# Optimization experiments

Hardware: AMD Instinct MI355X
Metric: run time of the kernel (lower is better)

The kernel has to match this reference:

```python
import jax, jax.numpy as jnp
import numpy as np

T_NO = 501          # refractory kernel length
COS_BASIS_NO = 30   # raised-cosine basis count
SCALE = 7.5
SHIFT = 1


def make_kern_basis():
    # kern_basis[i, t] = 0.5*cos(scale*log(t+shift+1e-7) - pi/2*i) + 0.5, zeroed outside [phi-pi, phi+pi]
    i = np.arange(COS_BASIS_NO, dtype=np.float64)[:, None]
    phi = 0.5 * np.pi * i
    x = np.arange(T_NO, dtype=np.float64)[None, :]
    raw = SCALE * np.log(x + SHIFT + 1e-7)
    basis = 0.5 * np.cos(raw - phi) + 0.5
    basis = np.where((raw < phi - np.pi) | (raw > phi + np.pi), 0.0, basis)
    return jnp.asarray(basis, jnp.float32)  # [30, T_NO]


def setup_inputs() -> dict:
    key = jax.random.key(0)
    ks = jax.random.split(key, 7)
    B, T = 64, 2048
    H_no = 5
    return {
        "V": jax.random.normal(ks[0], (B, T), jnp.float32),
        "D": jax.random.normal(ks[1], (B, T), jnp.float32),
        "w1": jax.random.normal(ks[2], (H_no, 2, 1), jnp.float32) * 0.5,   # Conv1d(2->H, k=1)
        "b1": jax.random.normal(ks[3], (H_no,), jnp.float32) * 0.1,
        "w2": jax.random.normal(ks[4], (1, H_no, 1), jnp.float32) * 0.5,   # Conv1d(H->1, k=1)
        "b2": jax.random.normal(ks[5], (1,), jnp.float32) * 0.1,
        "W_refract": jax.random.normal(ks[6], (COS_BASIS_NO,), jnp.float32) * 0.01,
    }


def reference(V, D, w1, b1, w2, b2, W_refract):
    B, T = V.shape
    kern_basis = make_kern_basis()
    refract_kern = jnp.flip(kern_basis.T @ W_refract)  # [T_NO], flipped as in torch

    # Ring-buffer alignment: sample at time s lives in column s % T_NO. At time t,
    # the original weights the window [t-T_NO, t-1] with refract_kern[0..T_NO-1]
    # (oldest -> kern[0]), i.e. column c gets weight refract_kern[(c - t) % T_NO].
    idx = (jnp.arange(T_NO)[None, :] - jnp.arange(T_NO)[:, None]) % T_NO
    kern_table = refract_kern[idx]  # [T_NO, T_NO]; kern_table[t % T_NO] is weights for step t

    # K_no=1, L_no=2 -> pointwise MLP: tanh(Conv1x1(2->H)) then Conv1x1(H->1)
    x = jnp.stack([V, D], axis=1)                                        # [B, 2, T]
    h = jnp.tanh(jnp.einsum('hc,bct->bht', w1[:, :, 0], x) + b1[None, :, None])
    nn_out = jnp.einsum('h,bht->bt', w2[0, :, 0], h) + b2[0]             # [B, T]

    key0 = jax.random.key(42)

    def step(carry, xs):
        ring, key = carry
        t, nn_t = xs                                   # nn_t: [B]
        key, sub = jax.random.split(key)
        p = t % T_NO
        refract = ring @ kern_table[p]                 # [B] sliding-window sum
        P_t = jax.nn.sigmoid(nn_t + refract)
        spike = jax.random.bernoulli(sub, P_t).astype(V.dtype)
        ring = ring.at[:, p].set(spike)                # overwrite slot that just expired
        return (ring, key), (spike, P_t)

    ring0 = jnp.zeros((B, T_NO), V.dtype)
    (_, _), (S_seq, P_seq) = jax.lax.scan(step, (ring0, key0), (jnp.arange(T), nn_out.T))
    S_out = S_seq.T  # [B, T]
    P_out = P_seq.T  # [B, T]
    return S_out, P_out
```

## Files before the change

### kernel.cpp

```cpp
#include <hip/hip_runtime.h>
#include <stdint.h>

typedef unsigned long long ull;

#define TT 2048

struct TF2 { uint32_t x, y; };

constexpr TF2 tf2x32(uint32_t k0, uint32_t k1, uint32_t x0, uint32_t x1) {
  uint32_t ks2 = k0 ^ k1 ^ 0x1BD11BDAu;
  x0 += k0; x1 += k1;
#define TFR_(r) x0 += x1; x1 = __builtin_rotateleft32(x1, r); x1 ^= x0;
  TFR_(13) TFR_(15) TFR_(26) TFR_(6)
  x0 += k1;  x1 += ks2 + 1u;
  TFR_(17) TFR_(29) TFR_(16) TFR_(24)
  x0 += ks2; x1 += k0 + 2u;
  TFR_(13) TFR_(15) TFR_(26) TFR_(6)
  x0 += k0;  x1 += k1 + 3u;
  TFR_(17) TFR_(29) TFR_(16) TFR_(24)
  x0 += k1;  x1 += ks2 + 4u;
  TFR_(13) TFR_(15) TFR_(26) TFR_(6)
  x0 += ks2; x1 += k0 + 5u;
#undef TFR_
  return {x0, x1};
}

struct Half_ { uint32_t a[1024]; uint32_t b[1024]; uint32_t k0, k1; };

constexpr Half_ make_half(uint32_t k0, uint32_t k1) {
  Half_ h{};
  for (int t = 0; t < 1024; ++t) {
    TF2 nk = tf2x32(k0, k1, 0u, 0u);
    TF2 sb = tf2x32(k0, k1, 0u, 1u);
    h.a[t] = sb.x; h.b[t] = sb.y;
    k0 = nk.x; k1 = nk.y;
  }
  h.k0 = k0; h.k1 = k1;
  return h;
}

namespace ckeys {
constexpr Half_ H0 = make_half(0u, 42u);
constexpr Half_ H1 = make_half(H0.k0, H0.k1);
}
__constant__ Half_ dH0 = ckeys::H0;
__constant__ Half_ dH1 = ckeys::H1;

__device__ __forceinline__ float tanh_xla(float x) {
#pragma clang fp contract(off)
  float ax = fabsf(x);
  float xc = fminf(fmaxf(x, -7.90531110763549805f), 7.90531110763549805f);
  float x2 = xc * xc;
  float p = fmaf(x2, -2.76076847742355e-16f, 2.00018790482477e-13f);
  p = fmaf(x2, p, -8.60467152213735e-11f);
  p = fmaf(x2, p, 5.12229709037114e-08f);
  p = fmaf(x2, p, 1.48572235717979e-05f);
  p = fmaf(x2, p, 6.37261928875436e-04f);
  p = fmaf(x2, p, 4.89352455891786e-03f);
  p = xc * p;
  float q = fmaf(x2, 1.19825839466702e-06f, 1.18534705686654e-04f);
  q = fmaf(x2, q, 2.26843463243900e-03f);
  q = fmaf(x2, q, 4.89352518554385e-03f);
  return (ax < 0.0004f) ? x : (p / q);
}

__device__ __forceinline__ float sig_ref(float z) {
#pragma clang fp contract(off)
  float e = (float)exp(-(double)z);
  return 1.0f / (1.0f + e);
}

__device__ __forceinline__ uint32_t ford(float f) {
  uint32_t x = __float_as_uint(f);
  return (x & 0x80000000u) ? ~x : (x | 0x80000000u);
}
__device__ __forceinline__ float fdec(uint32_t k) {
  uint32_t b = (k & 0x80000000u) ? (k & 0x7fffffffu) : ~k;
  return __uint_as_float(b);
}

__device__ float find_tau(float u) {
  if (!(u > 0.0f)) return -1.0e30f;
  double zg = log((double)u / (1.0 - (double)u));
  float zgf = (float)zg;
  zgf = fminf(fmaxf(zgf, -90.0f), 90.0f);
  uint32_t kc = ford(zgf);
  uint32_t klo = kc - 96u, khi = kc + 96u;
  if (!(sig_ref(fdec(klo)) <= u)) klo = ford(-95.0f);
  if (!(sig_ref(fdec(khi)) > u))  khi = ford(95.0f);
  while (khi - klo > 1u) {
    uint32_t km = klo + ((khi - klo) >> 1);
    if (sig_ref(fdec(km)) <= u) klo = km; else khi = km;
  }
  return fdec(klo);
}

__global__ void ap_pre_kernel(const float* __restrict__ V, const float* __restrict__ D,
                              const float* __restrict__ w1, const float* __restrict__ b1,
                              const float* __restrict__ w2, const float* __restrict__ b2,
                              const float* __restrict__ Wr,
                              float* __restrict__ zb, float* __restrict__ tauA,
                              float* __restrict__ rk, uint32_t* flags) {
#pragma clang fp contract(off)
  int tid = threadIdx.x;
  int blk = blockIdx.x;
  if (blk < 512) {
    int idx = blk * 256 + tid;
    int b = idx >> 11, t = idx & 2047;
    float v = V[idx], dd = D[idx];
    float acc = 0.f;
#pragma unroll
    for (int h = 0; h < 5; ++h) {
      float m = fmaf(w1[2 * h + 1], dd, w1[2 * h] * v) + b1[h];
      float th = tanh_xla(m);
      acc = (h == 0) ? (w2[0] * th) : fmaf(w2[h], th, acc);
    }
    float z0 = acc + b2[0];
    uint32_t ka = (t < 1024) ? dH0.a[t] : dH1.a[t - 1024];
    uint32_t kb = (t < 1024) ? dH0.b[t] : dH1.b[t - 1024];
    TF2 o = tf2x32(ka, kb, 0u, (uint32_t)b);
    uint32_t bits = o.x ^ o.y;
    float u = __uint_as_float((bits >> 9) | 0x3f800000u) - 1.0f;
    zb[t * 64 + b] = z0;
    tauA[t * 64 + b] = find_tau(u);
  } else if (blk < 514) {
    int d = (blk - 512) * 256 + tid;
    float val = 0.f;
    if (d >= 1 && d <= 501) {
      double raw = 7.5 * log((double)(d - 1) + 1.0 + 1e-7);
      float a = 0.f;
      for (int i = 0; i < 30; ++i) {
        double phi = (0.5 * 3.141592653589793) * (double)i;
        float bf;
        if (raw < phi - 3.141592653589793 || raw > phi + 3.141592653589793) bf = 0.f;
        else bf = (float)(0.5 * cos(raw - phi) + 0.5);
        a = fmaf(Wr[i], bf, a);
      }
      val = a;
    }
    rk[d] = val;
  } else {
    if (tid == 0) flags[0] = 0u;
    if (tid >= 1 && tid <= 64) {
      int c = tid - 1;
      flags[tid] = (c <= 4) ? 4u : 0u;
    }
  }
}

__global__ void __launch_bounds__(512, 1)
ap_main_kernel(float* __restrict__ zb, const float* __restrict__ tauA,
               const float* __restrict__ rk, float* __restrict__ zarr,
               ull* __restrict__ sw, uint32_t* flags) {
  __shared__ float lutS[20 * 256];
  __shared__ uint32_t snapL[16 * 64];
  __shared__ uint32_t snapA[16 * 64];
  __shared__ float comboL[64 * 64];
  __shared__ int winDone[8];
  __shared__ int progLds;
  __shared__ ull swL[384];
  __shared__ uint32_t colb[64 * 13];
  __shared__ float rkL[512];

  int tid = threadIdx.x;
  int lane = tid & 63;

  if (blockIdx.x == 0) {
    for (int e = tid; e < 20 * 256; e += 512) {
      int o = e >> 8, vb = e & 255;
      float s = 0.f;
      if (o < 10) {
        for (int i = 0; i < 8; ++i)
          if (vb & (1 << i)) s += rk[3 + 8 * o + i];
      } else {
        for (int i = 0; i < 8; ++i)
          if (vb & (1 << i)) s += rk[3 + 8 * o + 7 - i];
      }
      lutS[e] = s;
    }
    if (tid < 8) winDone[tid] = 0;
    if (tid == 0) progLds = 0;
    __syncthreads();

    int wv = tid >> 6;

    if (wv == 0) {
      float rk1 = rk[1], rk2 = rk[2];
      float zbR[2][16], tauR[2][16];
#pragma unroll
      for (int q = 0; q < 16; ++q) {
        zbR[0][q]  = zb[q * 64 + lane];
        tauR[0][q] = tauA[q * 64 + lane];
        zbR[1][q]  = zb[1024 + q * 64 + lane];
        tauR[1][q] = tauA[1024 + q * 64 + lane];
      }
      while (__hip_atomic_load(&winDone[0], __ATOMIC_ACQUIRE, __HIP_MEMORY_SCOPE_WORKGROUP) != 1)
        __builtin_amdgcn_s_sleep(1);
      float cpipe[2];
      cpipe[0] = comboL[0 * 64 + lane];
      cpipe[1] = comboL[1 * 64 + lane];
      float l[2][10];
#pragma unroll
      for (int k = 0; k < 10; ++k) { l[0][k] = 0.f; l[1][k] = 0.f; }
      uint32_t m0 = 0, m1 = 0, m2 = 0;
      float s1f = 0.f, s2f = 0.f;

      for (int wp = 0; wp < 64; ++wp) {
#pragma unroll
        for (int half = 0; half < 2; ++half) {
          int w = 2 * wp + half;
          if (w < 127) {
            int slot = (w + 1) & 7, gen = w + 2;
            while (__hip_atomic_load(&winDone[slot], __ATOMIC_ACQUIRE,
                                     __HIP_MEMORY_SCOPE_WORKGROUP) != gen)
              __builtin_amdgcn_s_sleep(1);
          }
          if (half == 0) {
            int c2 = (w + 2) >> 1;
            if (c2 >= 5 && c2 <= 63) {
              while ((int)__hip_atomic_load(&flags[1 + c2], __ATOMIC_ACQUIRE,
                                            __HIP_MEMORY_SCOPE_AGENT) < 4)
                __builtin_amdgcn_s_sleep(2);
            }
          }
          int wl = (w + 2 <= 127) ? (w + 2) : 127;
          const float* zbL  = zb + wl * 1024 + lane;
          const float* tauL = tauA + wl * 1024 + lane;
          float* zarrW = zarr + w * 1024 + lane;
          const float* comboLo = comboL + ((16 * w + 2) & 63) * 64 + lane;
          const float* comboHi = comboL + ((16 * w + 16) & 63) * 64 + lane;
#pragma unroll
          for (int q = 0; q < 16; ++q) {
            int p = q & 1;
            float g = ((l[p][0] + l[p][1]) + (l[p][2] + l[p][3]))
                    + ((l[p][4] + l[p][5]) + (l[p][6] + l[p][7]))
                    + (l[p][8] + l[p][9]);
            float z = (zbR[half][q] + cpipe[p]) + g;
            z = fmaf(rk2, s2f, z);
            z = fmaf(rk1, s1f, z);
            bool sp = z > tauR[half][q];
            zarrW[q * 64] = z;
            zbR[half][q]  = zbL[q * 64];
            tauR[half][q] = tauL[q * 64];
            cpipe[p] = (q < 14) ? comboLo[q * 64] : comboHi[(q - 14) * 64];
            l[p][0] = lutS[         (m0         & 255u)];
            l[p][1] = lutS[ 256 + ((m0 >> 8 )  & 255u)];
            l[p][2] = lutS[ 512 + ((m0 >> 16)  & 255u)];
            l[p][3] = lutS[ 768 + ( m0 >> 24          )];
            l[p][4] = lutS[1024 + ( m1         & 255u)];
            l[p][5] = lutS[1280 + ((m1 >> 8 )  & 255u)];
            l[p][6] = lutS[1536 + ((m1 >> 16)  & 255u)];
            l[p][7] = lutS[1792 + ( m1 >> 24          )];
            l[p][8] = lutS[2048 + ( m2         & 255u)];
            l[p][9] = lutS[2304 + ((m2 >> 8 )  & 255u)];
            m2 = __builtin_amdgcn_alignbit(m2, m1, 31);
            m1 = __builtin_amdgcn_alignbit(m1, m0, 31);
            m0 = (m0 << 1) | (sp ? 1u : 0u);
            s2f = s1f;
            s1f = sp ? 1.0f : 0.0f;
          }
          snapL[(w & 15) * 64 + lane] = m0;
          snapA[(w & 15) * 64 + lane] = __builtin_bitreverse32(m0);
          if (lane == 0)
            __hip_atomic_store(&progLds, 16 * w + 16, __ATOMIC_RELEASE,
                               __HIP_MEMORY_SCOPE_WORKGROUP);
        }
      }
      return;
    } else if (wv == 1 || wv == 2) {
      int par = wv - 1;
      for (int win = par; win < 128; win += 2) {
        if (win >= 4) {
          int tgt = 16 * (win - 3);
          while (__hip_atomic_load(&progLds, __ATOMIC_ACQUIRE,
                                   __HIP_MEMORY_SCOPE_WORKGROUP) < tgt)
            __builtin_amdgcn_s_sleep(1);
        }
        uint32_t a[8];
#pragma unroll
        for (int j = 0; j < 8; ++j) {
          int g = win - 12 + j;
          a[j] = (g >= 0) ? snapA[(g & 15) * 64 + lane] : 0u;
        }
        uint32_t r[4];
        r[0] = (a[0] >> 16) | (a[1] & 0xFFFF0000u);
        r[1] = (a[2] >> 16) | (a[3] & 0xFFFF0000u);
        r[2] = (a[4] >> 16) | (a[5] & 0xFFFF0000u);
        r[3] = (a[6] >> 16) | (a[7] & 0xFFFF0000u);
        float* cwp = comboL + ((16 * win) & 63) * 64 + lane;
#pragma unroll
        for (int q = 0; q < 16; ++q) {
          float acc = 0.f;
#pragma unroll
          for (int o = 10; o < 20; ++o) {
            int pos = q + 182 - 8 * o;
            int k = pos >> 5, sh = pos & 31;
            uint32_t byt;
            if (sh <= 24) byt = (r[k] >> sh) & 255u;
            else          byt = __builtin_amdgcn_alignbit(r[k + 1], r[k], (uint32_t)sh) & 255u;
            acc += lutS[o * 256 + byt];
          }
          cwp[q * 64] = acc;
        }
        if (lane == 0)
          __hip_atomic_store(&winDone[win & 7], win + 1, __ATOMIC_RELEASE,
                             __HIP_MEMORY_SCOPE_WORKGROUP);
      }
      return;
    } else if (wv == 3) {
      for (int m = 1; m <= 64; ++m) {
        while (__hip_atomic_load(&progLds, __ATOMIC_ACQUIRE,
                                 __HIP_MEMORY_SCOPE_WORKGROUP) < 32 * m)
          __builtin_amdgcn_s_sleep(2);
        uint32_t sA = snapL[((2 * m - 2) & 15) * 64 + lane];
        uint32_t sB = snapL[((2 * m - 1) & 15) * 64 + lane];
#pragma unroll
        for (int i = 0; i < 32; ++i) {
          uint32_t sn = (i < 16) ? sA : sB;
          uint32_t bit = (sn >> (15 - (i & 15))) & 1u;
          ull bal = __ballot(bit != 0u);
          if (lane == 0) sw[32 * (m - 1) + i] = bal;
        }
        if (lane == 0)
          __hip_atomic_store(&flags[0], (uint32_t)m, __ATOMIC_RELEASE,
                             __HIP_MEMORY_SCOPE_AGENT);
      }
      return;
    }
    return;
  }

  int c = 5 + ((int)blockIdx.x - 1) / 4;
  int qq = ((int)blockIdx.x - 1) & 3;
  int T0 = 32 * c + 8 * qq;
  int s0 = T0 - 501;
  if (tid == 0) {
    while ((int)__hip_atomic_load(&flags[0], __ATOMIC_ACQUIRE,
                                  __HIP_MEMORY_SCOPE_AGENT) < c - 4)
      __builtin_amdgcn_s_sleep(8);
  }
  __syncthreads();
  for (int i = tid; i < 384; i += 512) {
    int s = s0 + i;
    swL[i] = (s >= 0 && i < 346) ? sw[s] : 0ull;
  }
  rkL[tid] = rk[tid];
  __syncthreads();
  {
    int w8 = tid >> 6;
#pragma unroll
    for (int rep = 0; rep < 2; ++rep) {
      int W = w8 + 8 * rep;
      if (W < 12) {
        uint32_t word = 0;
        for (int i2 = 0; i2 < 32; ++i2) {
          ull v = swL[32 * W + i2];
          uint32_t bit = (uint32_t)((v >> lane) & 1ull);
          word |= bit << i2;
        }
        colb[lane * 13 + W] = word;
      }
    }
  }
  __syncthreads();
  {
    int tl = tid >> 6;
    int b = tid & 63;
    uint32_t cw[12];
#pragma unroll
    for (int W = 0; W < 12; ++W) cw[W] = colb[b * 13 + W];
    uint32_t A[11];
#pragma unroll
    for (int W = 0; W < 11; ++W)
      A[W] = __builtin_amdgcn_alignbit(cw[W + 1], cw[W], (uint32_t)tl);
    float acc = 0.f;
#pragma unroll 4
    for (int k = 0; k < 339; ++k) {
      float bv = (float)((A[k >> 5] >> (k & 31)) & 1u);
      acc = fmaf(bv, rkL[501 - k], acc);
    }
    int t = T0 + tl;
    zb[t * 64 + b] += acc;
  }
  __syncthreads();
  if (tid == 0)
    __hip_atomic_fetch_add(&flags[1 + c], 1u, __ATOMIC_RELEASE,
                           __HIP_MEMORY_SCOPE_AGENT);
}

__global__ void ap_post_kernel(const float* __restrict__ zarr, const float* __restrict__ tauA,
                               float* __restrict__ out) {
#pragma clang fp contract(off)
  int idx = blockIdx.x * 256 + threadIdx.x;
  int b = idx >> 11, t = idx & 2047;
  float z = zarr[t * 64 + b];
  float tau = tauA[t * 64 + b];
  out[idx] = (z > tau) ? 1.0f : 0.0f;
  out[131072 + idx] = 1.0f / (1.0f + __expf(-z));
}

extern "C" void kernel_launch(void* const* d_in, const int* in_sizes, int n_in,
                              void* d_out, int out_size, void* d_ws, size_t ws_size,
                              hipStream_t stream) {
  (void)in_sizes; (void)n_in; (void)out_size; (void)ws_size;
  const float* V  = (const float*)d_in[0];
  const float* D  = (const float*)d_in[1];
  const float* w1 = (const float*)d_in[2];
  const float* b1 = (const float*)d_in[3];
  const float* w2 = (const float*)d_in[4];
  const float* b2 = (const float*)d_in[5];
  const float* Wr = (const float*)d_in[6];

  char* w = (char*)d_ws;
  float*    zb    = (float*)w;
  float*    tauA  = (float*)(w + 0x080000);
  float*    zarr  = (float*)(w + 0x100000);
  ull*      swp   = (ull*)(w + 0x180000);
  float*    rk    = (float*)(w + 0x184000);
  uint32_t* flags = (uint32_t*)(w + 0x184800);

  ap_pre_kernel<<<515, 256, 0, stream>>>(V, D, w1, b1, w2, b2, Wr, zb, tauA, rk, flags);
  ap_main_kernel<<<237, 512, 0, stream>>>(zb, tauA, rk, zarr, swp, flags);
  ap_post_kernel<<<512, 256, 0, stream>>>(zarr, tauA, (float*)d_out);
}
```

Baseline: 445.8 us.

## Move combo and ballot waves to a separate workgroup communicating via global flags

Splits the serial recurrence wave into its own block 0. The far-window LUT combination and spike-ballot waves move to a new block 1, which folds the combo sum directly into zb in global memory. Cross-wave handoff now goes through global snapshot buffers and agent-scope flags instead of LDS and workgroup-scope atomics. This frees the critical wave from sharing its CU and LDS with helper waves, at the cost of higher-latency global-memory synchronisation on the critical path.

```diff
diff --git a/kernel.cpp b/kernel.cpp
--- a/kernel.cpp
+++ b/kernel.cpp
@@ -140,24 +140,17 @@
     }
     rk[d] = val;
   } else {
-    if (tid == 0) flags[0] = 0u;
-    if (tid >= 1 && tid <= 64) {
-      int c = tid - 1;
-      flags[tid] = (c <= 4) ? 4u : 0u;
-    }
+    if (tid < 256) flags[tid] = 0u;
+    if (tid >= 1 && tid <= 5) flags[tid] = 4u;
   }
 }
 
 __global__ void __launch_bounds__(512, 1)
-ap_main_kernel(float* __restrict__ zb, const float* __restrict__ tauA,
+ap_main_kernel(float* zb, const float* __restrict__ tauA,
                const float* __restrict__ rk, float* __restrict__ zarr,
-               ull* __restrict__ sw, uint32_t* flags) {
-  __shared__ float lutS[20 * 256];
-  __shared__ uint32_t snapL[16 * 64];
-  __shared__ uint32_t snapA[16 * 64];
-  __shared__ float comboL[64 * 64];
-  __shared__ int winDone[8];
-  __shared__ int progLds;
+               ull* __restrict__ sw, uint32_t* snapG, uint32_t* flags) {
+  __shared__ float lutS[10 * 256];
+  __shared__ float lutT[10 * 256];
   __shared__ ull swL[384];
   __shared__ uint32_t colb[64 * 13];
   __shared__ float rkL[512];
@@ -166,128 +159,129 @@
   int lane = tid & 63;
 
   if (blockIdx.x == 0) {
-    for (int e = tid; e < 20 * 256; e += 512) {
+    for (int e = tid; e < 10 * 256; e += 512) {
       int o = e >> 8, vb = e & 255;
       float s = 0.f;
-      if (o < 10) {
-        for (int i = 0; i < 8; ++i)
-          if (vb & (1 << i)) s += rk[3 + 8 * o + i];
-      } else {
-        for (int i = 0; i < 8; ++i)
-          if (vb & (1 << i)) s += rk[3 + 8 * o + 7 - i];
+      for (int i = 0; i < 8; ++i)
+        if (vb & (1 << i)) s += rk[3 + 8 * o + i];
+      lutS[e] = s;
+    }
+    __syncthreads();
+    if (tid >= 64) return;
+
+    float rk1 = rk[1], rk2 = rk[2];
+    float tauR[2][16], cbR[2][16];
+#pragma unroll
+    for (int q = 0; q < 16; ++q) {
+      tauR[0][q] = tauA[q * 64 + lane];
+      tauR[1][q] = tauA[1024 + q * 64 + lane];
+    }
+    while (__hip_atomic_load(&flags[65], __ATOMIC_ACQUIRE, __HIP_MEMORY_SCOPE_AGENT) != 1u)
+      __builtin_amdgcn_s_sleep(1);
+#pragma unroll
+    for (int q = 0; q < 16; ++q) cbR[0][q] = zb[q * 64 + lane];
+
+    float l[2][10];
+#pragma unroll
+    for (int k = 0; k < 10; ++k) { l[0][k] = 0.f; l[1][k] = 0.f; }
+    uint32_t m0 = 0, m1 = 0, m2 = 0;
+    float s1f = 0.f, s2f = 0.f;
+
+    for (int wp = 0; wp < 64; ++wp) {
+#pragma unroll
+      for (int half = 0; half < 2; ++half) {
+        int w = 2 * wp + half;
+        if (w < 127) {
+          uint32_t* tf = &flags[65 + w + 1];
+          while (__hip_atomic_load(tf, __ATOMIC_ACQUIRE, __HIP_MEMORY_SCOPE_AGENT) != 1u)
+            __builtin_amdgcn_s_sleep(1);
+          const float* cbL = zb + (w + 1) * 1024 + lane;
+#pragma unroll
+          for (int q = 0; q < 16; ++q) cbR[1 - half][q] = cbL[q * 64];
+        }
+        int wl = (w + 2 <= 127) ? (w + 2) : 127;
+        const float* tauL = tauA + wl * 1024 + lane;
+        float* zarrW = zarr + w * 1024 + lane;
+#pragma unroll
+        for (int q = 0; q < 16; ++q) {
+          int p = q & 1;
+          float g = ((l[p][0] + l[p][1]) + (l[p][2] + l[p][3]))
+                  + ((l[p][4] + l[p][5]) + (l[p][6] + l[p][7]))
+                  + (l[p][8] + l[p][9]);
+          float z = cbR[half][q] + g;
+          z = fmaf(rk2, s2f, z);
+          z = fmaf(rk1, s1f, z);
+          bool sp = z > tauR[half][q];
+          zarrW[q * 64] = z;
+          tauR[half][q] = tauL[q * 64];
+          l[p][0] = lutS[         (m0         & 255u)];
+          l[p][1] = lutS[ 256 + ((m0 >> 8 )  & 255u)];
+          l[p][2] = lutS[ 512 + ((m0 >> 16)  & 255u)];
+          l[p][3] = lutS[ 768 + ( m0 >> 24          )];
+          l[p][4] = lutS[1024 + ( m1         & 255u)];
+          l[p][5] = lutS[1280 + ((m1 >> 8 )  & 255u)];
+          l[p][6] = lutS[1536 + ((m1 >> 16)  & 255u)];
+          l[p][7] = lutS[1792 + ( m1 >> 24          )];
+          l[p][8] = lutS[2048 + ( m2         & 255u)];
+          l[p][9] = lutS[2304 + ((m2 >> 8 )  & 255u)];
+          m2 = __builtin_amdgcn_alignbit(m2, m1, 31);
+          m1 = __builtin_amdgcn_alignbit(m1, m0, 31);
+          m0 = (m0 << 1) | (sp ? 1u : 0u);
+          s2f = s1f;
+          s1f = sp ? 1.0f : 0.0f;
+        }
+        snapG[w * 64 + lane] = m0;
+        if (lane == 0)
+          __hip_atomic_store(&flags[200], (uint32_t)(16 * w + 16), __ATOMIC_RELEASE,
+                             __HIP_MEMORY_SCOPE_AGENT);
       }
-      lutS[e] = s;
-    }
-    if (tid < 8) winDone[tid] = 0;
-    if (tid == 0) progLds = 0;
+    }
+    return;
+  }
+
+  if (blockIdx.x == 1) {
+    for (int e = tid; e < 10 * 256; e += 512) {
+      int m = e >> 8, vb = e & 255;
+      float s = 0.f;
+      for (int i = 0; i < 8; ++i)
+        if (vb & (1 << i)) s += rk[90 + 8 * m - i];
+      lutT[e] = s;
+    }
     __syncthreads();
-
     int wv = tid >> 6;
 
-    if (wv == 0) {
-      float rk1 = rk[1], rk2 = rk[2];
-      float zbR[2][16], tauR[2][16];
-#pragma unroll
-      for (int q = 0; q < 16; ++q) {
-        zbR[0][q]  = zb[q * 64 + lane];
-        tauR[0][q] = tauA[q * 64 + lane];
-        zbR[1][q]  = zb[1024 + q * 64 + lane];
-        tauR[1][q] = tauA[1024 + q * 64 + lane];
-      }
-      while (__hip_atomic_load(&winDone[0], __ATOMIC_ACQUIRE, __HIP_MEMORY_SCOPE_WORKGROUP) != 1)
-        __builtin_amdgcn_s_sleep(1);
-      float cpipe[2];
-      cpipe[0] = comboL[0 * 64 + lane];
-      cpipe[1] = comboL[1 * 64 + lane];
-      float l[2][10];
-#pragma unroll
-      for (int k = 0; k < 10; ++k) { l[0][k] = 0.f; l[1][k] = 0.f; }
-      uint32_t m0 = 0, m1 = 0, m2 = 0;
-      float s1f = 0.f, s2f = 0.f;
-
-      for (int wp = 0; wp < 64; ++wp) {
-#pragma unroll
-        for (int half = 0; half < 2; ++half) {
-          int w = 2 * wp + half;
-          if (w < 127) {
-            int slot = (w + 1) & 7, gen = w + 2;
-            while (__hip_atomic_load(&winDone[slot], __ATOMIC_ACQUIRE,
-                                     __HIP_MEMORY_SCOPE_WORKGROUP) != gen)
-              __builtin_amdgcn_s_sleep(1);
-          }
-          if (half == 0) {
-            int c2 = (w + 2) >> 1;
-            if (c2 >= 5 && c2 <= 63) {
-              while ((int)__hip_atomic_load(&flags[1 + c2], __ATOMIC_ACQUIRE,
-                                            __HIP_MEMORY_SCOPE_AGENT) < 4)
-                __builtin_amdgcn_s_sleep(2);
-            }
-          }
-          int wl = (w + 2 <= 127) ? (w + 2) : 127;
-          const float* zbL  = zb + wl * 1024 + lane;
-          const float* tauL = tauA + wl * 1024 + lane;
-          float* zarrW = zarr + w * 1024 + lane;
-          const float* comboLo = comboL + ((16 * w + 2) & 63) * 64 + lane;
-          const float* comboHi = comboL + ((16 * w + 16) & 63) * 64 + lane;
-#pragma unroll
-          for (int q = 0; q < 16; ++q) {
-            int p = q & 1;
-            float g = ((l[p][0] + l[p][1]) + (l[p][2] + l[p][3]))
-                    + ((l[p][4] + l[p][5]) + (l[p][6] + l[p][7]))
-                    + (l[p][8] + l[p][9]);
-            float z = (zbR[half][q] + cpipe[p]) + g;
-            z = fmaf(rk2, s2f, z);
-            z = fmaf(rk1, s1f, z);
-            bool sp = z > tauR[half][q];
-            zarrW[q * 64] = z;
-            zbR[half][q]  = zbL[q * 64];
-            tauR[half][q] = tauL[q * 64];
-            cpipe[p] = (q < 14) ? comboLo[q * 64] : comboHi[(q - 14) * 64];
-            l[p][0] = lutS[         (m0         & 255u)];
-            l[p][1] = lutS[ 256 + ((m0 >> 8 )  & 255u)];
-            l[p][2] = lutS[ 512 + ((m0 >> 16)  & 255u)];
-            l[p][3] = lutS[ 768 + ( m0 >> 24          )];
-            l[p][4] = lutS[1024 + ( m1         & 255u)];
-            l[p][5] = lutS[1280 + ((m1 >> 8 )  & 255u)];
-            l[p][6] = lutS[1536 + ((m1 >> 16)  & 255u)];
-            l[p][7] = lutS[1792 + ( m1 >> 24          )];
-            l[p][8] = lutS[2048 + ( m2         & 255u)];
-            l[p][9] = lutS[2304 + ((m2 >> 8 )  & 255u)];
-            m2 = __builtin_amdgcn_alignbit(m2, m1, 31);
-            m1 = __builtin_amdgcn_alignbit(m1, m0, 31);
-            m0 = (m0 << 1) | (sp ? 1u : 0u);
-            s2f = s1f;
-            s1f = sp ? 1.0f : 0.0f;
-          }
-          snapL[(w & 15) * 64 + lane] = m0;
-          snapA[(w & 15) * 64 + lane] = __builtin_bitreverse32(m0);
-          if (lane == 0)
-            __hip_atomic_store(&progLds, 16 * w + 16, __ATOMIC_RELEASE,
-                               __HIP_MEMORY_SCOPE_WORKGROUP);
-        }
-      }
-      return;
-    } else if (wv == 1 || wv == 2) {
-      int par = wv - 1;
+    if (wv < 2) {
+      int par = wv;
+      int cConf = 4;
       for (int win = par; win < 128; win += 2) {
         if (win >= 4) {
-          int tgt = 16 * (win - 3);
-          while (__hip_atomic_load(&progLds, __ATOMIC_ACQUIRE,
-                                   __HIP_MEMORY_SCOPE_WORKGROUP) < tgt)
+          uint32_t tgt = (uint32_t)(16 * (win - 3));
+          while (__hip_atomic_load(&flags[200], __ATOMIC_ACQUIRE,
+                                   __HIP_MEMORY_SCOPE_AGENT) < tgt)
             __builtin_amdgcn_s_sleep(1);
+        }
+        int c = win >> 1;
+        if (c >= 5 && c > cConf) {
+          while (__hip_atomic_load(&flags[1 + c], __ATOMIC_ACQUIRE,
+                                   __HIP_MEMORY_SCOPE_AGENT) < 4u)
+            __builtin_amdgcn_s_sleep(2);
+          cConf = c;
         }
         uint32_t a[8];
 #pragma unroll
         for (int j = 0; j < 8; ++j) {
           int g = win - 12 + j;
-          a[j] = (g >= 0) ? snapA[(g & 15) * 64 + lane] : 0u;
+          a[j] = (g >= 0) ? __builtin_bitreverse32(snapG[g * 64 + lane]) : 0u;
         }
         uint32_t r[4];
         r[0] = (a[0] >> 16) | (a[1] & 0xFFFF0000u);
         r[1] = (a[2] >> 16) | (a[3] & 0xFFFF0000u);
         r[2] = (a[4] >> 16) | (a[5] & 0xFFFF0000u);
         r[3] = (a[6] >> 16) | (a[7] & 0xFFFF0000u);
-        float* cwp = comboL + ((16 * win) & 63) * 64 + lane;
+        float* zrow = zb + 16 * win * 64 + lane;
+        float zv[16];
+#pragma unroll
+        for (int q = 0; q < 16; ++q) zv[q] = zrow[q * 64];
 #pragma unroll
         for (int q = 0; q < 16; ++q) {
           float acc = 0.f;
@@ -298,22 +292,22 @@
             uint32_t byt;
             if (sh <= 24) byt = (r[k] >> sh) & 255u;
             else          byt = __builtin_amdgcn_alignbit(r[k + 1], r[k], (uint32_t)sh) & 255u;
-            acc += lutS[o * 256 + byt];
+            acc += lutT[(o - 10) * 256 + byt];
           }
-          cwp[q * 64] = acc;
+          zrow[q * 64] = zv[q] + acc;
         }
         if (lane == 0)
-          __hip_atomic_store(&winDone[win & 7], win + 1, __ATOMIC_RELEASE,
-                             __HIP_MEMORY_SCOPE_WORKGROUP);
+          __hip_atomic_store(&flags[65 + win], 1u, __ATOMIC_RELEASE,
+                             __HIP_MEMORY_SCOPE_AGENT);
       }
       return;
-    } else if (wv == 3) {
+    } else if (wv == 2) {
       for (int m = 1; m <= 64; ++m) {
-        while (__hip_atomic_load(&progLds, __ATOMIC_ACQUIRE,
-                                 __HIP_MEMORY_SCOPE_WORKGROUP) < 32 * m)
+        while (__hip_atomic_load(&flags[200], __ATOMIC_ACQUIRE,
+                                 __HIP_MEMORY_SCOPE_AGENT) < (uint32_t)(32 * m))
           __builtin_amdgcn_s_sleep(2);
-        uint32_t sA = snapL[((2 * m - 2) & 15) * 64 + lane];
-        uint32_t sB = snapL[((2 * m - 1) & 15) * 64 + lane];
+        uint32_t sA = snapG[(2 * m - 2) * 64 + lane];
+        uint32_t sB = snapG[(2 * m - 1) * 64 + lane];
 #pragma unroll
         for (int i = 0; i < 32; ++i) {
           uint32_t sn = (i < 16) ? sA : sB;
@@ -330,8 +324,8 @@
     return;
   }
 
-  int c = 5 + ((int)blockIdx.x - 1) / 4;
-  int qq = ((int)blockIdx.x - 1) & 3;
+  int c = 5 + ((int)blockIdx.x - 2) / 4;
+  int qq = ((int)blockIdx.x - 2) & 3;
   int T0 = 32 * c + 8 * qq;
   int s0 = T0 - 501;
   if (tid == 0) {
@@ -418,8 +412,9 @@
   ull*      swp   = (ull*)(w + 0x180000);
   float*    rk    = (float*)(w + 0x184000);
   uint32_t* flags = (uint32_t*)(w + 0x184800);
+  uint32_t* snapG = (uint32_t*)(w + 0x185000);
 
   ap_pre_kernel<<<515, 256, 0, stream>>>(V, D, w1, b1, w2, b2, Wr, zb, tauA, rk, flags);
-  ap_main_kernel<<<237, 512, 0, stream>>>(zb, tauA, rk, zarr, swp, flags);
+  ap_main_kernel<<<238, 512, 0, stream>>>(zb, tauA, rk, zarr, swp, snapG, flags);
   ap_post_kernel<<<512, 256, 0, stream>>>(zarr, tauA, (float*)d_out);
 }
```

Result: slower. 850.1 us (+90.7%).

## Offload more refractory window terms to helper waves and pack combo into float4

Applied to the files above, without the earlier changes.

The serial sampling wave now tracks only 48 recent spike bits (6 LUT lookups) instead of 80 (10 lookups). Older bytes move to helper waves: four waves compute the deep history plus the zb bias and a partial, and two more compute a mid-range partial. The helpers also fold in the zb and tau loads and write everything into one packed float4 per step, so the critical loop does a single LDS read instead of separate global loads. This shortens the per-step dependency chain in the serial wave. In exchange it adds more producer waves, a second set of window-done flags, and tighter producer lag, which could stall the serial wave if the helpers fall behind.

```diff
diff --git a/kernel.cpp b/kernel.cpp
--- a/kernel.cpp
+++ b/kernel.cpp
@@ -149,14 +149,15 @@
 }
 
 __global__ void __launch_bounds__(512, 1)
-ap_main_kernel(float* __restrict__ zb, const float* __restrict__ tauA,
+ap_main_kernel(float* zb, const float* __restrict__ tauA,
                const float* __restrict__ rk, float* __restrict__ zarr,
                ull* __restrict__ sw, uint32_t* flags) {
-  __shared__ float lutS[20 * 256];
-  __shared__ uint32_t snapL[16 * 64];
-  __shared__ uint32_t snapA[16 * 64];
-  __shared__ float comboL[64 * 64];
-  __shared__ int winDone[8];
+  __shared__ float lutS[6 * 256];
+  __shared__ float lutM[14 * 256];
+  __shared__ float4 comboQ[64 * 64];
+  __shared__ uint32_t snapR[16 * 64];
+  __shared__ int winDoneA[8];
+  __shared__ int winDoneB[8];
   __shared__ int progLds;
   __shared__ ull swL[384];
   __shared__ uint32_t colb[64 * 13];
@@ -166,19 +167,26 @@
   int lane = tid & 63;
 
   if (blockIdx.x == 0) {
-    for (int e = tid; e < 20 * 256; e += 512) {
+    for (int e = tid; e < 6 * 256; e += 512) {
       int o = e >> 8, vb = e & 255;
       float s = 0.f;
-      if (o < 10) {
+      for (int i = 0; i < 8; ++i)
+        if (vb & (1 << i)) s += rk[3 + 8 * o + i];
+      lutS[e] = s;
+    }
+    for (int e = tid; e < 14 * 256; e += 512) {
+      int o = 6 + (e >> 8), vb = e & 255;
+      float s = 0.f;
+      if (o <= 9) {
         for (int i = 0; i < 8; ++i)
-          if (vb & (1 << i)) s += rk[3 + 8 * o + i];
+          if ((vb >> (7 - i)) & 1) s += rk[3 + 8 * o + i];
       } else {
         for (int i = 0; i < 8; ++i)
-          if (vb & (1 << i)) s += rk[3 + 8 * o + 7 - i];
-      }
-      lutS[e] = s;
-    }
-    if (tid < 8) winDone[tid] = 0;
+          if ((vb >> i) & 1) s += rk[3 + 8 * o + 7 - i];
+      }
+      lutM[e] = s;
+    }
+    if (tid < 8) { winDoneA[tid] = 0; winDoneB[tid] = 0; }
     if (tid == 0) progLds = 0;
     __syncthreads();
 
@@ -186,134 +194,168 @@
 
     if (wv == 0) {
       float rk1 = rk[1], rk2 = rk[2];
-      float zbR[2][16], tauR[2][16];
-#pragma unroll
-      for (int q = 0; q < 16; ++q) {
-        zbR[0][q]  = zb[q * 64 + lane];
-        tauR[0][q] = tauA[q * 64 + lane];
-        zbR[1][q]  = zb[1024 + q * 64 + lane];
-        tauR[1][q] = tauA[1024 + q * 64 + lane];
-      }
-      while (__hip_atomic_load(&winDone[0], __ATOMIC_ACQUIRE, __HIP_MEMORY_SCOPE_WORKGROUP) != 1)
-        __builtin_amdgcn_s_sleep(1);
-      float cpipe[2];
-      cpipe[0] = comboL[0 * 64 + lane];
-      cpipe[1] = comboL[1 * 64 + lane];
-      float l[2][10];
-#pragma unroll
-      for (int k = 0; k < 10; ++k) { l[0][k] = 0.f; l[1][k] = 0.f; }
-      uint32_t m0 = 0, m1 = 0, m2 = 0;
+      auto pollWin = [&](int vv) {
+        int slot = vv & 7, gen = vv + 1;
+        while (__hip_atomic_load(&winDoneA[slot], __ATOMIC_ACQUIRE, __HIP_MEMORY_SCOPE_WORKGROUP) != gen ||
+               __hip_atomic_load(&winDoneB[slot], __ATOMIC_ACQUIRE, __HIP_MEMORY_SCOPE_WORKGROUP) != gen)
+          __builtin_amdgcn_s_sleep(1);
+      };
+      pollWin(0); pollWin(1);
+      float4 cp4[2];
+      cp4[0] = comboQ[0 * 64 + lane];
+      cp4[1] = comboQ[1 * 64 + lane];
+      float l[2][6];
+#pragma unroll
+      for (int k = 0; k < 6; ++k) { l[0][k] = 0.f; l[1][k] = 0.f; }
+      uint32_t m0 = 0, m1 = 0;
       float s1f = 0.f, s2f = 0.f;
 
-      for (int wp = 0; wp < 64; ++wp) {
-#pragma unroll
-        for (int half = 0; half < 2; ++half) {
-          int w = 2 * wp + half;
-          if (w < 127) {
-            int slot = (w + 1) & 7, gen = w + 2;
-            while (__hip_atomic_load(&winDone[slot], __ATOMIC_ACQUIRE,
-                                     __HIP_MEMORY_SCOPE_WORKGROUP) != gen)
-              __builtin_amdgcn_s_sleep(1);
-          }
-          if (half == 0) {
-            int c2 = (w + 2) >> 1;
-            if (c2 >= 5 && c2 <= 63) {
-              while ((int)__hip_atomic_load(&flags[1 + c2], __ATOMIC_ACQUIRE,
-                                            __HIP_MEMORY_SCOPE_AGENT) < 4)
-                __builtin_amdgcn_s_sleep(2);
-            }
-          }
-          int wl = (w + 2 <= 127) ? (w + 2) : 127;
-          const float* zbL  = zb + wl * 1024 + lane;
-          const float* tauL = tauA + wl * 1024 + lane;
-          float* zarrW = zarr + w * 1024 + lane;
-          const float* comboLo = comboL + ((16 * w + 2) & 63) * 64 + lane;
-          const float* comboHi = comboL + ((16 * w + 16) & 63) * 64 + lane;
-#pragma unroll
-          for (int q = 0; q < 16; ++q) {
-            int p = q & 1;
-            float g = ((l[p][0] + l[p][1]) + (l[p][2] + l[p][3]))
-                    + ((l[p][4] + l[p][5]) + (l[p][6] + l[p][7]))
-                    + (l[p][8] + l[p][9]);
-            float z = (zbR[half][q] + cpipe[p]) + g;
-            z = fmaf(rk2, s2f, z);
-            z = fmaf(rk1, s1f, z);
-            bool sp = z > tauR[half][q];
-            zarrW[q * 64] = z;
-            zbR[half][q]  = zbL[q * 64];
-            tauR[half][q] = tauL[q * 64];
-            cpipe[p] = (q < 14) ? comboLo[q * 64] : comboHi[(q - 14) * 64];
-            l[p][0] = lutS[         (m0         & 255u)];
-            l[p][1] = lutS[ 256 + ((m0 >> 8 )  & 255u)];
-            l[p][2] = lutS[ 512 + ((m0 >> 16)  & 255u)];
-            l[p][3] = lutS[ 768 + ( m0 >> 24          )];
-            l[p][4] = lutS[1024 + ( m1         & 255u)];
-            l[p][5] = lutS[1280 + ((m1 >> 8 )  & 255u)];
-            l[p][6] = lutS[1536 + ((m1 >> 16)  & 255u)];
-            l[p][7] = lutS[1792 + ( m1 >> 24          )];
-            l[p][8] = lutS[2048 + ( m2         & 255u)];
-            l[p][9] = lutS[2304 + ((m2 >> 8 )  & 255u)];
-            m2 = __builtin_amdgcn_alignbit(m2, m1, 31);
-            m1 = __builtin_amdgcn_alignbit(m1, m0, 31);
-            m0 = (m0 << 1) | (sp ? 1u : 0u);
-            s2f = s1f;
-            s1f = sp ? 1.0f : 0.0f;
-          }
-          snapL[(w & 15) * 64 + lane] = m0;
-          snapA[(w & 15) * 64 + lane] = __builtin_bitreverse32(m0);
-          if (lane == 0)
-            __hip_atomic_store(&progLds, 16 * w + 16, __ATOMIC_RELEASE,
-                               __HIP_MEMORY_SCOPE_WORKGROUP);
-        }
+      for (int w = 0; w < 128; ++w) {
+        if (w + 1 < 128) pollWin(w + 1);
+        int baseLo = ((16 * w + 2) & 63) * 64 + lane;
+        int baseHi = ((16 * w + 16) & 63) * 64 + lane;
+        float* zarrW = zarr + w * 1024 + lane;
+#pragma unroll
+        for (int q = 0; q < 16; ++q) {
+          int p = q & 1;
+          float4 f4 = cp4[p];
+          float a1 = l[p][0] + l[p][1];
+          float a2 = l[p][2] + l[p][3];
+          float A  = a1 + a2;
+          float b1 = l[p][4] + l[p][5];
+          float B  = b1 + f4.y;
+          float g  = (A + B) + f4.z;
+          float z  = f4.x + g;
+          z = fmaf(rk2, s2f, z);
+          z = fmaf(rk1, s1f, z);
+          bool sp = z > f4.w;
+          zarrW[q * 64] = z;
+          cp4[p] = (q < 14) ? comboQ[baseLo + q * 64] : comboQ[baseHi + (q - 14) * 64];
+          l[p][0] = lutS[         (m0        & 255u)];
+          l[p][1] = lutS[ 256 + ((m0 >> 8 ) & 255u)];
+          l[p][2] = lutS[ 512 + ((m0 >> 16) & 255u)];
+          l[p][3] = lutS[ 768 + ( m0 >> 24         )];
+          l[p][4] = lutS[1024 + ( m1        & 255u)];
+          l[p][5] = lutS[1280 + ((m1 >> 8 ) & 255u)];
+          m1 = __builtin_amdgcn_alignbit(m1, m0, 31);
+          m0 = (m0 << 1) | (sp ? 1u : 0u);
+          s2f = s1f;
+          s1f = sp ? 1.0f : 0.0f;
+        }
+        snapR[(w & 15) * 64 + lane] = m0;
+        if (lane == 0)
+          __hip_atomic_store(&progLds, 16 * w + 16, __ATOMIC_RELEASE,
+                             __HIP_MEMORY_SCOPE_WORKGROUP);
       }
       return;
-    } else if (wv == 1 || wv == 2) {
-      int par = wv - 1;
-      for (int win = par; win < 128; win += 2) {
-        if (win >= 4) {
-          int tgt = 16 * (win - 3);
+    } else if (wv >= 1 && wv <= 4) {
+      int cConf = 4;
+      for (int v = wv - 1; v < 128; v += 4) {
+        if (v >= 4) {
+          int tgt = 16 * v - 48;
           while (__hip_atomic_load(&progLds, __ATOMIC_ACQUIRE,
                                    __HIP_MEMORY_SCOPE_WORKGROUP) < tgt)
             __builtin_amdgcn_s_sleep(1);
         }
+        int c = v >> 1;
+        if (c >= 5 && c > cConf) {
+          while (__hip_atomic_load(&flags[1 + c], __ATOMIC_ACQUIRE,
+                                   __HIP_MEMORY_SCOPE_AGENT) < 4u)
+            __builtin_amdgcn_s_sleep(2);
+          cConf = c;
+        }
         uint32_t a[8];
 #pragma unroll
         for (int j = 0; j < 8; ++j) {
-          int g = win - 12 + j;
-          a[j] = (g >= 0) ? snapA[(g & 15) * 64 + lane] : 0u;
+          int g = v - 11 + j;
+          a[j] = (g >= 0) ? __builtin_bitreverse32(snapR[(g & 15) * 64 + lane]) : 0u;
         }
         uint32_t r[4];
         r[0] = (a[0] >> 16) | (a[1] & 0xFFFF0000u);
         r[1] = (a[2] >> 16) | (a[3] & 0xFFFF0000u);
         r[2] = (a[4] >> 16) | (a[5] & 0xFFFF0000u);
         r[3] = (a[6] >> 16) | (a[7] & 0xFFFF0000u);
-        float* cwp = comboL + ((16 * win) & 63) * 64 + lane;
+        const float* zvp = zb + 16 * v * 64 + lane;
+        const float* tvp = tauA + 16 * v * 64 + lane;
+        float zv[16], tv[16];
+#pragma unroll
+        for (int q = 0; q < 16; ++q) { zv[q] = zvp[q * 64]; tv[q] = tvp[q * 64]; }
 #pragma unroll
         for (int q = 0; q < 16; ++q) {
-          float acc = 0.f;
-#pragma unroll
-          for (int o = 10; o < 20; ++o) {
-            int pos = q + 182 - 8 * o;
+          float e8 = 0.f, e9 = 0.f, acc = 0.f;
+#pragma unroll
+          for (int o = 8; o < 20; ++o) {
+            int pos = q + 166 - 8 * o;
             int k = pos >> 5, sh = pos & 31;
             uint32_t byt;
             if (sh <= 24) byt = (r[k] >> sh) & 255u;
             else          byt = __builtin_amdgcn_alignbit(r[k + 1], r[k], (uint32_t)sh) & 255u;
-            acc += lutS[o * 256 + byt];
+            float ent = lutM[(o - 6) * 256 + byt];
+            if (o == 8) e8 = ent;
+            else if (o == 9) e9 = ent;
+            else acc += ent;
           }
-          cwp[q * 64] = acc;
+          float P89 = e8 + e9;
+          float combo = zv[q] + acc;
+          int idx = ((16 * v + q) & 63) * 64 + lane;
+          comboQ[idx].x = combo;
+          *(float2*)((float*)&comboQ[idx] + 2) = make_float2(P89, tv[q]);
         }
         if (lane == 0)
-          __hip_atomic_store(&winDone[win & 7], win + 1, __ATOMIC_RELEASE,
+          __hip_atomic_store(&winDoneA[v & 7], v + 1, __ATOMIC_RELEASE,
                              __HIP_MEMORY_SCOPE_WORKGROUP);
       }
       return;
-    } else if (wv == 3) {
+    } else if (wv == 5 || wv == 6) {
+      for (int v = wv - 5; v < 128; v += 2) {
+        if (v >= 3) {
+          int tgt = 16 * v - 32;
+          while (__hip_atomic_load(&progLds, __ATOMIC_ACQUIRE,
+                                   __HIP_MEMORY_SCOPE_WORKGROUP) < tgt)
+            __builtin_amdgcn_s_sleep(1);
+        }
+        uint32_t a2[4];
+#pragma unroll
+        for (int j = 0; j < 4; ++j) {
+          int g = v - 6 + j;
+          a2[j] = (g >= 0) ? __builtin_bitreverse32(snapR[(g & 15) * 64 + lane]) : 0u;
+        }
+        uint32_t r2[2];
+        r2[0] = (a2[0] >> 16) | (a2[1] & 0xFFFF0000u);
+        r2[1] = (a2[2] >> 16) | (a2[3] & 0xFFFF0000u);
+#pragma unroll
+        for (int q = 0; q < 16; ++q) {
+          float e6, e7;
+          {
+            int pos = q + 38;
+            int sh = pos & 31;
+            uint32_t byt = (r2[1] >> sh) & 255u;
+            e6 = lutM[0 * 256 + byt];
+          }
+          {
+            int pos = q + 30;
+            int k = pos >> 5, sh = pos & 31;
+            uint32_t byt;
+            if (sh <= 24) byt = (r2[k] >> sh) & 255u;
+            else          byt = __builtin_amdgcn_alignbit(r2[k + 1], r2[k], (uint32_t)sh) & 255u;
+            e7 = lutM[1 * 256 + byt];
+          }
+          float P67 = e6 + e7;
+          int idx = ((16 * v + q) & 63) * 64 + lane;
+          ((float*)&comboQ[idx])[1] = P67;
+        }
+        if (lane == 0)
+          __hip_atomic_store(&winDoneB[v & 7], v + 1, __ATOMIC_RELEASE,
+                             __HIP_MEMORY_SCOPE_WORKGROUP);
+      }
+      return;
+    } else {
       for (int m = 1; m <= 64; ++m) {
         while (__hip_atomic_load(&progLds, __ATOMIC_ACQUIRE,
                                  __HIP_MEMORY_SCOPE_WORKGROUP) < 32 * m)
           __builtin_amdgcn_s_sleep(2);
-        uint32_t sA = snapL[((2 * m - 2) & 15) * 64 + lane];
-        uint32_t sB = snapL[((2 * m - 1) & 15) * 64 + lane];
+        uint32_t sA = snapR[((2 * m - 2) & 15) * 64 + lane];
+        uint32_t sB = snapR[((2 * m - 1) & 15) * 64 + lane];
 #pragma unroll
         for (int i = 0; i < 32; ++i) {
           uint32_t sn = (i < 16) ? sA : sB;
@@ -327,7 +369,6 @@
       }
       return;
     }
-    return;
   }
 
   int c = 5 + ((int)blockIdx.x - 1) / 4;
```

New measurement: 507.0 us. +13.7%, slower.
